# Kernel optimization log

Measured on AMD Instinct MI355X. Metric: run time of the kernel, lower is better.

The kernel has to match this reference:

```python
import jax, jax.numpy as jnp
import numpy as np

B, LQ = 16, 2048
EMB1, EMB2, HDIM, NHEAD = 1024, 768, 1024, 16


def setup_inputs() -> dict:
    key = jax.random.key(0)
    ks = jax.random.split(key, 8)
    s1 = 1.0 / np.sqrt(EMB1)
    s2 = 1.0 / np.sqrt(EMB2)
    return {
        "emb1": jax.random.normal(ks[0], (B, LQ, EMB1), jnp.float32),
        "emb2": jax.random.normal(ks[1], (B, EMB2), jnp.float32),
        "Wq": jax.random.uniform(ks[2], (HDIM, EMB1), jnp.float32, -s1, s1),
        "bq": jax.random.uniform(ks[3], (HDIM,), jnp.float32, -s1, s1),
        "Wk": jax.random.uniform(ks[4], (HDIM, EMB2), jnp.float32, -s2, s2),
        "bk": jax.random.uniform(ks[5], (HDIM,), jnp.float32, -s2, s2),
        "Wv": jax.random.uniform(ks[6], (HDIM, EMB2), jnp.float32, -s2, s2),
        "bv": jax.random.uniform(ks[7], (HDIM,), jnp.float32, -s2, s2),
        "n_head": NHEAD,
    }


def reference(emb1, emb2, Wq, bq, Wk, bk, Wv, bv, n_head):
    b, lq, _ = emb1.shape
    hdim = Wq.shape[0]
    dh = hdim // n_head
    # Q: [b, lq, hdim] -> [b, H, lq, dh]
    q = (jnp.einsum("bqe,he->bqh", emb1, Wq) + bq).reshape(b, lq, n_head, dh).transpose(0, 2, 1, 3)
    # K, V from per-batch vector: [b, hdim] -> [b, H, 1, dh]
    k = (emb2 @ Wk.T + bk).reshape(b, 1, n_head, dh).transpose(0, 2, 1, 3)
    v = (emb2 @ Wv.T + bv).reshape(b, 1, n_head, dh).transpose(0, 2, 1, 3)
    # att: [b, H, lq, 1] (no softmax, no scaling)
    att = jnp.einsum("bhqd,bhkd->bhqk", q, k)
    # sigmoid gate broadcast-multiplied with V: [b,H,lq,1]*[b,H,1,dh] -> [b,H,lq,dh]
    out = jax.nn.sigmoid(att) * v
    # back to [b, lq, hdim]; torch .squeeze(1) is a no-op for lq > 1
    return out.transpose(0, 2, 1, 3).reshape(b, lq, hdim)
```

## Files before the change

### kernel.cpp

```cpp
#include <hip/hip_runtime.h>
#include <hip/hip_fp16.h>
#include <cstdint>


__global__ __launch_bounds__(256) void kv_kernel(
    const float* __restrict__ emb2, const float* __restrict__ Wk,
    const float* __restrict__ bk,   const float* __restrict__ Wv,
    const float* __restrict__ bv,   float* __restrict__ ws)
{
    const int kind  = blockIdx.y;
    const int htile = blockIdx.x;
    const float* W    = kind ? Wv : Wk;
    const float* bias = kind ? bv : bk;
    float* outp = ws + (kind ? 16384 : 0);

    __shared__ float se2[16 * 772];
    const int t = threadIdx.x;
    #pragma unroll 4
    for (int i = 0; i < 48; ++i) {
        int idx = i * 256 + t;
        int b = idx / 768;
        int e = idx - b * 768;
        se2[b * 772 + e] = emb2[idx];
    }
    __syncthreads();

    const int hl = t >> 4, b = t & 15;
    const int h  = htile * 16 + hl;
    float acc = bias[h];
    const float4* W4 = (const float4*)(W + (size_t)h * 768);
    const float*  e2 = &se2[b * 772];
    #pragma unroll 4
    for (int j = 0; j < 192; ++j) {
        float4 w = W4[j];
        float4 a = *(const float4*)(e2 + j * 4);
        acc += w.x * a.x + w.y * a.y + w.z * a.z + w.w * a.w;
    }
    outp[b * 1024 + h] = acc;
}

__global__ __launch_bounds__(256) void fold_kernel(
    const float* __restrict__ Wq, const float* __restrict__ bq,
    float* __restrict__ ws)
{
    const int h  = blockIdx.x;
    const int et = blockIdx.y;
    const float* kvec = ws;
    float* attb = ws + 32768;
    __half* wqk = (__half*)((char*)ws + 132096);

    __shared__ float kk[16 * 64];
    const int t = threadIdx.x;
    {
        int idx0 = t;
        #pragma unroll
        for (int i = 0; i < 4; ++i) {
            int idx = i * 256 + idx0;
            int b = idx >> 6, d = idx & 63;
            kk[b * 64 + d] = kvec[b * 1024 + h * 64 + d];
        }
    }
    __syncthreads();

    if (et == 0 && t < 16) {
        float s = 0.f;
        #pragma unroll 8
        for (int d = 0; d < 64; ++d) s += kk[t * 64 + d] * bq[h * 64 + d];
        attb[t * 16 + h] = s;
    }

    const int e = et * 256 + t;
    float acc[16];
    #pragma unroll
    for (int b = 0; b < 16; ++b) acc[b] = 0.f;

    const float* Wcol = Wq + (size_t)(h * 64) * 1024 + e;
    for (int d = 0; d < 64; ++d) {
        float wv = Wcol[(size_t)d * 1024];
        #pragma unroll
        for (int b = 0; b < 16; ++b) acc[b] += kk[b * 64 + d] * wv;
    }
    #pragma unroll
    for (int b = 0; b < 16; ++b)
        wqk[(size_t)(b * 16 + h) * 1024 + e] = __float2half_rn(acc[b]);
}

__global__ __launch_bounds__(256) void att_kernel(
    const float* __restrict__ emb1, const float* __restrict__ ws,
    float* __restrict__ out)
{
    const int bx = blockIdx.x;
    const int b  = blockIdx.y;
    const float*  vvec = ws + 16384 + b * 1024;
    const float*  attb = ws + 32768 + b * 16;
    const __half* wqk  = (const __half*)((const char*)ws + 132096) + (size_t)b * 16384;

    __shared__ __half sw[16 * 64 * 16];

    const int t = threadIdx.x;
    #pragma unroll
    for (int i = 0; i < 8; ++i) {
        int c   = i * 256 + t;
        int h   = c >> 7;
        int seg = (c >> 5) & 3;
        int lp  = c & 31;
        uint4 vld = *(const uint4*)(wqk + h * 1024 + seg * 256 + lp * 8);
        *(uint2*)&sw[(h * 64 + lp * 2    ) * 16 + seg * 4] = make_uint2(vld.x, vld.y);
        *(uint2*)&sw[(h * 64 + lp * 2 + 1) * 16 + seg * 4] = make_uint2(vld.z, vld.w);
    }
    __syncthreads();

    const int w    = t >> 6;
    const int lane = t & 63;
    const int g    = lane >> 4;

    float4 vv[4];
    #pragma unroll
    for (int s = 0; s < 4; ++s) vv[s] = *(const float4*)(vvec + s * 256 + lane * 4);

    const int l0 = lane & 1, l1 = (lane >> 1) & 1, l2 = (lane >> 2) & 1, l3 = (lane >> 3) & 1;
    const int hmine = (l0 << 3) | (l1 << 2) | (l2 << 1) | l3;
    const float attb_l = attb[hmine];

    int src[4];
    #pragma unroll
    for (int s = 0; s < 4; ++s)
        src[s] = ((g & 1) << 3) | ((g >> 1) << 2) | ((s & 1) << 1) | (s >> 1);

    const int row0 = bx * 32 + w * 8;
    const float* Abase = emb1 + ((size_t)b * 2048 + row0) * 1024 + lane * 4;
    float*       Obase = out  + ((size_t)b * 2048 + row0) * 1024 + lane * 4;
    const __half2* wl2 = (const __half2*)(sw + lane * 16);

    for (int r = 0; r < 8; ++r) {
        const float* A = Abase + r * 1024;
        float4 a0 = *(const float4*)(A);
        float4 a1 = *(const float4*)(A + 256);
        float4 a2 = *(const float4*)(A + 512);
        float4 a3 = *(const float4*)(A + 768);

        float acc[16];
        #pragma unroll
        for (int h = 0; h < 16; ++h) {
            const __half2* wp = wl2 + h * 512;
            float2 f0 = __half22float2(wp[0]);
            float2 f1 = __half22float2(wp[1]);
            float2 f2 = __half22float2(wp[2]);
            float2 f3 = __half22float2(wp[3]);
            float2 f4 = __half22float2(wp[4]);
            float2 f5 = __half22float2(wp[5]);
            float2 f6 = __half22float2(wp[6]);
            float2 f7 = __half22float2(wp[7]);
            float s;
            s  = f0.x * a0.x + f0.y * a0.y + f1.x * a0.z + f1.y * a0.w;
            s += f2.x * a1.x + f2.y * a1.y + f3.x * a1.z + f3.y * a1.w;
            s += f4.x * a2.x + f4.y * a2.y + f5.x * a2.z + f5.y * a2.w;
            s += f6.x * a3.x + f6.y * a3.y + f7.x * a3.z + f7.y * a3.w;
            acc[h] = s;
        }

        {
            const bool hi = l0;
            #pragma unroll
            for (int i = 0; i < 8; ++i) {
                float send = hi ? acc[i] : acc[i + 8];
                float keep = hi ? acc[i + 8] : acc[i];
                acc[i] = keep + __shfl_xor(send, 1);
            }
        }
        {
            const bool hi = l1;
            #pragma unroll
            for (int i = 0; i < 4; ++i) {
                float send = hi ? acc[i] : acc[i + 4];
                float keep = hi ? acc[i + 4] : acc[i];
                acc[i] = keep + __shfl_xor(send, 2);
            }
        }
        {
            const bool hi = l2;
            #pragma unroll
            for (int i = 0; i < 2; ++i) {
                float send = hi ? acc[i] : acc[i + 2];
                float keep = hi ? acc[i + 2] : acc[i];
                acc[i] = keep + __shfl_xor(send, 4);
            }
        }
        {
            const bool hi = l3;
            float send = hi ? acc[0] : acc[1];
            float keep = hi ? acc[1] : acc[0];
            acc[0] = keep + __shfl_xor(send, 8);
        }
        float r0 = acc[0];
        r0 += __shfl_xor(r0, 16);
        r0 += __shfl_xor(r0, 32);

        float att  = r0 + attb_l;
        float gate = 1.0f / (1.0f + __expf(-att));

        float* O = Obase + (size_t)r * 1024;
        #pragma unroll
        for (int s = 0; s < 4; ++s) {
            float gs = __shfl(gate, src[s]);
            float4 o;
            o.x = gs * vv[s].x; o.y = gs * vv[s].y;
            o.z = gs * vv[s].z; o.w = gs * vv[s].w;
            *(float4*)(O + s * 256) = o;
        }
    }
}

extern "C" void kernel_launch(void* const* d_in, const int* in_sizes, int n_in,
                              void* d_out, int out_size, void* d_ws, size_t ws_size,
                              hipStream_t stream) {
    const float* emb1 = (const float*)d_in[0];
    const float* emb2 = (const float*)d_in[1];
    const float* Wq   = (const float*)d_in[2];
    const float* bq   = (const float*)d_in[3];
    const float* Wk   = (const float*)d_in[4];
    const float* bk   = (const float*)d_in[5];
    const float* Wv   = (const float*)d_in[6];
    const float* bv   = (const float*)d_in[7];
    float* out = (float*)d_out;
    float* ws  = (float*)d_ws;

    kv_kernel  <<<dim3(64, 2),  256, 0, stream>>>(emb2, Wk, bk, Wv, bv, ws);
    fold_kernel<<<dim3(16, 4),  256, 0, stream>>>(Wq, bq, ws);
    att_kernel <<<dim3(64, 16), 256, 0, stream>>>(emb1, ws, out);
}
```

Baseline: 304.6 us.

## Restructure all three kernels: split-K kv, per-batch fold, register-resident weights in att

The kv kernel splits the 768-long reduction across four warps and reduces through shared memory, using more blocks. The fold kernel gives each batch its own block and uses coalesced float4 row reads of Wq. The att kernel gives each warp 4 heads with their folded weights held in registers instead of shared memory, processes all 32 rows per warp with a software-prefetched next row, and writes output with nontemporal stores. This aims to remove the shared-memory weight traffic and the staging overhead and to raise parallelism in the small kernels. In exchange it uses more registers (launch bounds 3) and shortens the shuffle reduction, but every warp now rereads the full emb1 row.

```diff
diff --git a/kernel.cpp b/kernel.cpp
--- a/kernel.cpp
+++ b/kernel.cpp
@@ -2,6 +2,8 @@
 #include <hip/hip_fp16.h>
 #include <cstdint>
 
+
+typedef float f4v __attribute__((ext_vector_type(4)));
 
 __global__ __launch_bounds__(256) void kv_kernel(
     const float* __restrict__ emb2, const float* __restrict__ Wk,
@@ -14,199 +16,161 @@
     const float* bias = kind ? bv : bk;
     float* outp = ws + (kind ? 16384 : 0);
 
-    __shared__ float se2[16 * 772];
-    const int t = threadIdx.x;
-    #pragma unroll 4
-    for (int i = 0; i < 48; ++i) {
-        int idx = i * 256 + t;
-        int b = idx / 768;
-        int e = idx - b * 768;
-        se2[b * 772 + e] = emb2[idx];
-    }
-    __syncthreads();
+    const int t  = threadIdx.x;
+    const int es = t >> 6;
+    const int hl = (t >> 4) & 3;
+    const int b  = t & 15;
+    const int h  = htile * 4 + hl;
 
-    const int hl = t >> 4, b = t & 15;
-    const int h  = htile * 16 + hl;
-    float acc = bias[h];
-    const float4* W4 = (const float4*)(W + (size_t)h * 768);
-    const float*  e2 = &se2[b * 772];
-    #pragma unroll 4
-    for (int j = 0; j < 192; ++j) {
+    const float4* W4 = (const float4*)(W + (size_t)h * 768) + es * 48;
+    const float4* E4 = (const float4*)(emb2 + (size_t)b * 768) + es * 48;
+
+    float acc = 0.f;
+    #pragma unroll 8
+    for (int j = 0; j < 48; ++j) {
         float4 w = W4[j];
-        float4 a = *(const float4*)(e2 + j * 4);
+        float4 a = E4[j];
         acc += w.x * a.x + w.y * a.y + w.z * a.z + w.w * a.w;
     }
-    outp[b * 1024 + h] = acc;
+
+    __shared__ float red[256];
+    red[t] = acc;
+    __syncthreads();
+    if (t < 64) {
+        float s = red[t] + red[t + 64] + red[t + 128] + red[t + 192] + bias[h];
+        outp[b * 1024 + h] = s;
+    }
 }
 
 __global__ __launch_bounds__(256) void fold_kernel(
     const float* __restrict__ Wq, const float* __restrict__ bq,
     float* __restrict__ ws)
 {
-    const int h  = blockIdx.x;
-    const int et = blockIdx.y;
+    const int h = blockIdx.x;
+    const int b = blockIdx.y;
     const float* kvec = ws;
     float* attb = ws + 32768;
     __half* wqk = (__half*)((char*)ws + 132096);
 
-    __shared__ float kk[16 * 64];
     const int t = threadIdx.x;
-    {
-        int idx0 = t;
-        #pragma unroll
-        for (int i = 0; i < 4; ++i) {
-            int idx = i * 256 + idx0;
-            int b = idx >> 6, d = idx & 63;
-            kk[b * 64 + d] = kvec[b * 1024 + h * 64 + d];
-        }
+    __shared__ float kk[64];
+    if (t < 64) {
+        float kvl = kvec[b * 1024 + h * 64 + t];
+        kk[t] = kvl;
+        float s = kvl * bq[h * 64 + t];
+        s += __shfl_xor(s, 1);  s += __shfl_xor(s, 2);
+        s += __shfl_xor(s, 4);  s += __shfl_xor(s, 8);
+        s += __shfl_xor(s, 16); s += __shfl_xor(s, 32);
+        if (t == 0) attb[b * 16 + h] = s;
     }
     __syncthreads();
 
-    if (et == 0 && t < 16) {
-        float s = 0.f;
-        #pragma unroll 8
-        for (int d = 0; d < 64; ++d) s += kk[t * 64 + d] * bq[h * 64 + d];
-        attb[t * 16 + h] = s;
+    float4 acc = make_float4(0.f, 0.f, 0.f, 0.f);
+    const float4* Wrow = (const float4*)(Wq + (size_t)(h * 64) * 1024) + t;
+    #pragma unroll 8
+    for (int d = 0; d < 64; ++d) {
+        float4 w = Wrow[(size_t)d * 256];
+        float kd = kk[d];
+        acc.x += kd * w.x; acc.y += kd * w.y;
+        acc.z += kd * w.z; acc.w += kd * w.w;
     }
-
-    const int e = et * 256 + t;
-    float acc[16];
-    #pragma unroll
-    for (int b = 0; b < 16; ++b) acc[b] = 0.f;
-
-    const float* Wcol = Wq + (size_t)(h * 64) * 1024 + e;
-    for (int d = 0; d < 64; ++d) {
-        float wv = Wcol[(size_t)d * 1024];
-        #pragma unroll
-        for (int b = 0; b < 16; ++b) acc[b] += kk[b * 64 + d] * wv;
-    }
-    #pragma unroll
-    for (int b = 0; b < 16; ++b)
-        wqk[(size_t)(b * 16 + h) * 1024 + e] = __float2half_rn(acc[b]);
+    union { __half2 h2[2]; uint2 u; } pk;
+    pk.h2[0] = __floats2half2_rn(acc.x, acc.y);
+    pk.h2[1] = __floats2half2_rn(acc.z, acc.w);
+    *(uint2*)(wqk + (size_t)(b * 16 + h) * 1024 + t * 4) = pk.u;
 }
 
-__global__ __launch_bounds__(256) void att_kernel(
+__global__ __launch_bounds__(256, 3) void att_kernel(
     const float* __restrict__ emb1, const float* __restrict__ ws,
     float* __restrict__ out)
 {
     const int bx = blockIdx.x;
     const int b  = blockIdx.y;
+    const int t    = threadIdx.x;
+    const int w    = t >> 6;
+    const int lane = t & 63;
+
     const float*  vvec = ws + 16384 + b * 1024;
     const float*  attb = ws + 32768 + b * 16;
     const __half* wqk  = (const __half*)((const char*)ws + 132096) + (size_t)b * 16384;
 
-    __shared__ __half sw[16 * 64 * 16];
+    float4 wf[4][4];
+    #pragma unroll
+    for (int hh = 0; hh < 4; ++hh) {
+        const __half* wrow = wqk + (w * 4 + hh) * 1024;
+        #pragma unroll
+        for (int s = 0; s < 4; ++s) {
+            const __half2* p = (const __half2*)(wrow + s * 256 + lane * 4);
+            float2 lo = __half22float2(p[0]);
+            float2 hi = __half22float2(p[1]);
+            wf[hh][s] = make_float4(lo.x, lo.y, hi.x, hi.y);
+        }
+    }
 
-    const int t = threadIdx.x;
+    const int   hloc   = ((lane & 1) << 1) | ((lane >> 1) & 1);
+    const float attb_l = attb[w * 4 + hloc];
+    const int   gsrc   = ((lane >> 5) & 1) | (((lane >> 4) & 1) << 1);
+
+    const float4 vv = *(const float4*)(vvec + w * 256 + lane * 4);
+
+    const int row0 = bx * 32;
+    const float* Abase = emb1 + ((size_t)b * 2048 + row0) * 1024 + lane * 4;
+    float*       Obase = out  + ((size_t)b * 2048 + row0) * 1024 + w * 256 + lane * 4;
+
+    float4 a[4], an[4];
     #pragma unroll
-    for (int i = 0; i < 8; ++i) {
-        int c   = i * 256 + t;
-        int h   = c >> 7;
-        int seg = (c >> 5) & 3;
-        int lp  = c & 31;
-        uint4 vld = *(const uint4*)(wqk + h * 1024 + seg * 256 + lp * 8);
-        *(uint2*)&sw[(h * 64 + lp * 2    ) * 16 + seg * 4] = make_uint2(vld.x, vld.y);
-        *(uint2*)&sw[(h * 64 + lp * 2 + 1) * 16 + seg * 4] = make_uint2(vld.z, vld.w);
-    }
-    __syncthreads();
+    for (int s = 0; s < 4; ++s) a[s] = *(const float4*)(Abase + s * 256);
 
-    const int w    = t >> 6;
-    const int lane = t & 63;
-    const int g    = lane >> 4;
+    for (int r = 0; r < 32; ++r) {
+        if (r < 31) {
+            const float* An = Abase + (size_t)(r + 1) * 1024;
+            #pragma unroll
+            for (int s = 0; s < 4; ++s) an[s] = *(const float4*)(An + s * 256);
+        }
 
-    float4 vv[4];
-    #pragma unroll
-    for (int s = 0; s < 4; ++s) vv[s] = *(const float4*)(vvec + s * 256 + lane * 4);
-
-    const int l0 = lane & 1, l1 = (lane >> 1) & 1, l2 = (lane >> 2) & 1, l3 = (lane >> 3) & 1;
-    const int hmine = (l0 << 3) | (l1 << 2) | (l2 << 1) | l3;
-    const float attb_l = attb[hmine];
-
-    int src[4];
-    #pragma unroll
-    for (int s = 0; s < 4; ++s)
-        src[s] = ((g & 1) << 3) | ((g >> 1) << 2) | ((s & 1) << 1) | (s >> 1);
-
-    const int row0 = bx * 32 + w * 8;
-    const float* Abase = emb1 + ((size_t)b * 2048 + row0) * 1024 + lane * 4;
-    float*       Obase = out  + ((size_t)b * 2048 + row0) * 1024 + lane * 4;
-    const __half2* wl2 = (const __half2*)(sw + lane * 16);
-
-    for (int r = 0; r < 8; ++r) {
-        const float* A = Abase + r * 1024;
-        float4 a0 = *(const float4*)(A);
-        float4 a1 = *(const float4*)(A + 256);
-        float4 a2 = *(const float4*)(A + 512);
-        float4 a3 = *(const float4*)(A + 768);
-
-        float acc[16];
+        float acc[4] = {0.f, 0.f, 0.f, 0.f};
         #pragma unroll
-        for (int h = 0; h < 16; ++h) {
-            const __half2* wp = wl2 + h * 512;
-            float2 f0 = __half22float2(wp[0]);
-            float2 f1 = __half22float2(wp[1]);
-            float2 f2 = __half22float2(wp[2]);
-            float2 f3 = __half22float2(wp[3]);
-            float2 f4 = __half22float2(wp[4]);
-            float2 f5 = __half22float2(wp[5]);
-            float2 f6 = __half22float2(wp[6]);
-            float2 f7 = __half22float2(wp[7]);
-            float s;
-            s  = f0.x * a0.x + f0.y * a0.y + f1.x * a0.z + f1.y * a0.w;
-            s += f2.x * a1.x + f2.y * a1.y + f3.x * a1.z + f3.y * a1.w;
-            s += f4.x * a2.x + f4.y * a2.y + f5.x * a2.z + f5.y * a2.w;
-            s += f6.x * a3.x + f6.y * a3.y + f7.x * a3.z + f7.y * a3.w;
-            acc[h] = s;
+        for (int s = 0; s < 4; ++s) {
+            float4 as = a[s];
+            #pragma unroll
+            for (int hh = 0; hh < 4; ++hh) {
+                float4 ww = wf[hh][s];
+                acc[hh] += ww.x * as.x + ww.y * as.y + ww.z * as.z + ww.w * as.w;
+            }
         }
 
         {
-            const bool hi = l0;
-            #pragma unroll
-            for (int i = 0; i < 8; ++i) {
-                float send = hi ? acc[i] : acc[i + 8];
-                float keep = hi ? acc[i + 8] : acc[i];
-                acc[i] = keep + __shfl_xor(send, 1);
-            }
-        }
-        {
-            const bool hi = l1;
-            #pragma unroll
-            for (int i = 0; i < 4; ++i) {
-                float send = hi ? acc[i] : acc[i + 4];
-                float keep = hi ? acc[i + 4] : acc[i];
-                acc[i] = keep + __shfl_xor(send, 2);
-            }
-        }
-        {
-            const bool hi = l2;
+            const bool hi = lane & 1;
             #pragma unroll
             for (int i = 0; i < 2; ++i) {
                 float send = hi ? acc[i] : acc[i + 2];
                 float keep = hi ? acc[i + 2] : acc[i];
-                acc[i] = keep + __shfl_xor(send, 4);
+                acc[i] = keep + __shfl_xor(send, 1);
             }
         }
+        float r0;
         {
-            const bool hi = l3;
+            const bool hi = lane & 2;
             float send = hi ? acc[0] : acc[1];
             float keep = hi ? acc[1] : acc[0];
-            acc[0] = keep + __shfl_xor(send, 8);
+            r0 = keep + __shfl_xor(send, 2);
         }
-        float r0 = acc[0];
+        r0 += __shfl_xor(r0, 4);
+        r0 += __shfl_xor(r0, 8);
         r0 += __shfl_xor(r0, 16);
         r0 += __shfl_xor(r0, 32);
 
-        float att  = r0 + attb_l;
-        float gate = 1.0f / (1.0f + __expf(-att));
+        const float att  = r0 + attb_l;
+        const float gate = 1.0f / (1.0f + __expf(-att));
+        const float g    = __shfl(gate, gsrc);
 
-        float* O = Obase + (size_t)r * 1024;
-        #pragma unroll
-        for (int s = 0; s < 4; ++s) {
-            float gs = __shfl(gate, src[s]);
-            float4 o;
-            o.x = gs * vv[s].x; o.y = gs * vv[s].y;
-            o.z = gs * vv[s].z; o.w = gs * vv[s].w;
-            *(float4*)(O + s * 256) = o;
+        f4v o;
+        o.x = g * vv.x; o.y = g * vv.y; o.z = g * vv.z; o.w = g * vv.w;
+        __builtin_nontemporal_store(o, (f4v*)(Obase + (size_t)r * 1024));
+
+        if (r < 31) {
+            #pragma unroll
+            for (int s = 0; s < 4; ++s) a[s] = an[s];
         }
     }
 }
@@ -225,7 +189,7 @@
     float* out = (float*)d_out;
     float* ws  = (float*)d_ws;
 
-    kv_kernel  <<<dim3(64, 2),  256, 0, stream>>>(emb2, Wk, bk, Wv, bv, ws);
-    fold_kernel<<<dim3(16, 4),  256, 0, stream>>>(Wq, bq, ws);
+    kv_kernel  <<<dim3(256, 2), 256, 0, stream>>>(emb2, Wk, bk, Wv, bv, ws);
+    fold_kernel<<<dim3(16, 16), 256, 0, stream>>>(Wq, bq, ws);
     att_kernel <<<dim3(64, 16), 256, 0, stream>>>(emb1, ws, out);
 }
```

Result: faster. 289.3 us (-5.0%).
